# Optimization experiments

Hardware: AMD Instinct MI355X
Metric: run time of the kernel (lower is better)

Reference implementation:

```python
import jax, jax.numpy as jnp
import numpy as np

B, C, H, W = 16, 384, 128, 128
RED = 6                      # reduction
CH = C // RED                # 64
CF = C // 2 + 1              # 193 rfft bins


def setup_inputs() -> dict:
    key = jax.random.key(0)
    ks = jax.random.split(key, 9)
    sc = 0.05
    return {
        "x":   jax.random.normal(ks[0], (B, C, H, W), dtype=jnp.float32),
        "W1":  jax.random.normal(ks[1], (CH, C, 3, 3), dtype=jnp.float32) * sc,
        "b1":  jax.random.normal(ks[2], (CH,), dtype=jnp.float32) * sc,
        "W2":  jax.random.normal(ks[3], (C, CH, 3, 3), dtype=jnp.float32) * sc,
        "b2":  jax.random.normal(ks[4], (C,), dtype=jnp.float32) * sc,
        "Ws1": jax.random.normal(ks[5], (CF, C), dtype=jnp.float32) * sc,
        "bs1": jax.random.normal(ks[6], (CF,), dtype=jnp.float32) * sc,
        "Ws2": jax.random.normal(ks[7], (CF, C), dtype=jnp.float32) * sc,
        "bs2": jax.random.normal(ks[8], (CF,), dtype=jnp.float32) * sc,
    }


def reference(x, W1, b1, W2, b2, Ws1, bs1, Ws2, bs2):
    b, c = x.shape[0], x.shape[1]
    # global average pool -> [b, c]
    y0 = jnp.mean(x, axis=(2, 3))
    # fc: 3x3 convs on 1x1 spatial input (pad=1) reduce to center-tap matmuls
    h = jax.nn.relu(y0 @ W1[:, :, 1, 1].T + b1)            # [b, c//red]
    y = jax.nn.sigmoid(h @ W2[:, :, 1, 1].T + b2)          # [b, c]
    # seq1 / seq2: 1x1 convs on [b, c, 1, 1]
    s1 = jax.nn.relu(y @ Ws1.T + bs1)                      # [b, c//2+1]
    s2 = jax.nn.relu(y @ Ws2.T + bs2)                      # [b, c//2+1]
    # rfft2 over (1, c) spatial dims == 1-D rfft over channel axis
    yf = jnp.fft.rfft(y, axis=-1)                          # [b, c//2+1] complex
    amp = jnp.abs(yf) * s1
    pha = jnp.angle(yf) * s2
    rec = jax.lax.complex(amp * jnp.cos(pha), amp * jnp.sin(pha))
    xr = jnp.fft.irfft(rec, n=c, axis=-1)                  # [b, c]
    out = (xr * y)[:, :, None, None]                       # [b, c, 1, 1]
    return out
```

## Files before the change

### kernel.cpp

```cpp
#include <hip/hip_runtime.h>

#define BB 16
#define CC 384
#define CH 64
#define CF 193
#define HW 16384

__global__ __launch_bounds__(256) void pool_kernel(const float4* __restrict__ x,
                                                   float* __restrict__ y0) {
    const int plane = blockIdx.x;
    const float4* p = x + (size_t)plane * (HW / 4);
    const int t = threadIdx.x;

    float s = 0.f;
#pragma unroll
    for (int r = 0; r < HW / 4 / 256; ++r) {
        float4 v = p[t + 256 * r];
        s += v.x + v.y + v.z + v.w;
    }

#pragma unroll
    for (int off = 32; off > 0; off >>= 1) s += __shfl_down(s, off);

    __shared__ float red[4];
    const int wid = t >> 6, lane = t & 63;
    if (lane == 0) red[wid] = s;
    __syncthreads();
    if (t == 0) {
        float tot = red[0] + red[1] + red[2] + red[3];
        y0[plane] = tot * (1.0f / (float)HW);
    }
}

__global__ __launch_bounds__(384) void head_kernel(
    const float* __restrict__ y0g,
    const float* __restrict__ W1,  const float* __restrict__ b1,
    const float* __restrict__ W2,  const float* __restrict__ b2,
    const float* __restrict__ Ws1, const float* __restrict__ bs1,
    const float* __restrict__ Ws2, const float* __restrict__ bs2,
    float* __restrict__ out)
{
    __shared__ float y0[CC], h[CH], y[CC];
    __shared__ float ct[CC], st[CC];
    __shared__ float rr[CF], ri[CF];

    const int b = blockIdx.x, t = threadIdx.x;

    y0[t] = y0g[b * CC + t];
    {
        float ang = (float)t * (6.283185307179586f / (float)CC);
        float sv, cv;
        sincosf(ang, &sv, &cv);
        st[t] = sv; ct[t] = cv;
    }
    __syncthreads();

    if (t < CH) {
        float acc = b1[t];
        const float* w = W1 + (size_t)t * CC * 9 + 4;
        for (int c = 0; c < CC; ++c) acc += y0[c] * w[c * 9];
        h[t] = fmaxf(acc, 0.f);
    }
    __syncthreads();

    {
        float acc = b2[t];
        const float* w = W2 + (size_t)t * CH * 9 + 4;
        for (int j = 0; j < CH; ++j) acc += h[j] * w[j * 9];
        y[t] = 1.f / (1.f + expf(-acc));
    }
    __syncthreads();

    if (t < CF) {
        const float* w1r = Ws1 + (size_t)t * CC;
        const float* w2r = Ws2 + (size_t)t * CC;
        float a1 = bs1[t], a2 = bs2[t];
        float re = 0.f, im = 0.f;
        int m = 0;
        for (int c = 0; c < CC; ++c) {
            float yc = y[c];
            a1 += yc * w1r[c];
            a2 += yc * w2r[c];
            re += yc * ct[m];
            im -= yc * st[m];
            m += t; if (m >= CC) m -= CC;
        }
        a1 = fmaxf(a1, 0.f);
        a2 = fmaxf(a2, 0.f);
        float amp = sqrtf(re * re + im * im) * a1;
        float pha = atan2f(im, re) * a2;
        float sp, cp;
        sincosf(pha, &sp, &cp);
        rr[t] = amp * cp;
        ri[t] = amp * sp;
    }
    __syncthreads();

    {
        float acc = 0.f;
        int m = 0;
        for (int k = 1; k < 192; ++k) {
            m += t; if (m >= CC) m -= CC;
            acc += rr[k] * ct[m] - ri[k] * st[m];
        }
        float nyq = (t & 1) ? -rr[192] : rr[192];
        float xr = (rr[0] + 2.f * acc + nyq) * (1.0f / (float)CC);
        out[b * CC + t] = xr * y[t];
    }
}

extern "C" void kernel_launch(void* const* d_in, const int* in_sizes, int n_in,
                              void* d_out, int out_size, void* d_ws, size_t ws_size,
                              hipStream_t stream) {
    const float4* x = (const float4*)d_in[0];
    const float* W1  = (const float*)d_in[1];
    const float* b1  = (const float*)d_in[2];
    const float* W2  = (const float*)d_in[3];
    const float* b2  = (const float*)d_in[4];
    const float* Ws1 = (const float*)d_in[5];
    const float* bs1 = (const float*)d_in[6];
    const float* Ws2 = (const float*)d_in[7];
    const float* bs2 = (const float*)d_in[8];
    float* out = (float*)d_out;

    float* y0 = (float*)d_ws;

    pool_kernel<<<BB * CC, 256, 0, stream>>>(x, y0);
    head_kernel<<<BB, 384, 0, stream>>>(y0, W1, b1, W2, b2, Ws1, bs1, Ws2, bs2, out);
}
```

Measured before the change: 614.4 us.

## Split head into batched fc1, fc2, spectral and irfft kernels

Replaces the single per-batch head kernel, which ran only 16 blocks, with four kernels. Each kernel maps batch onto thread lanes and output features onto blocks, so weight rows are shared across the batch. Pooled activations are stored channel-major so batch lanes read contiguously. This is meant to remove the serial latency of the low-parallelism head. In exchange it adds extra kernel launches and global round-trips for the intermediates.

```diff
diff --git a/kernel.cpp b/kernel.cpp
--- a/kernel.cpp
+++ b/kernel.cpp
@@ -6,10 +6,12 @@
 #define CF 193
 #define HW 16384
 
+#define TWO_PI_OVER_CC (6.283185307179586f / (float)CC)
+
 __global__ __launch_bounds__(256) void pool_kernel(const float4* __restrict__ x,
-                                                   float* __restrict__ y0) {
-    const int plane = blockIdx.x;
-    const float4* p = x + (size_t)plane * (HW / 4);
+                                                   float* __restrict__ y0T) {
+    const int c = blockIdx.x, b = blockIdx.y;
+    const float4* p = x + (size_t)(b * CC + c) * (HW / 4);
     const int t = threadIdx.x;
 
     float s = 0.f;
@@ -18,7 +20,6 @@
         float4 v = p[t + 256 * r];
         s += v.x + v.y + v.z + v.w;
     }
-
 #pragma unroll
     for (int off = 32; off > 0; off >>= 1) s += __shfl_down(s, off);
 
@@ -28,91 +29,111 @@
     __syncthreads();
     if (t == 0) {
         float tot = red[0] + red[1] + red[2] + red[3];
-        y0[plane] = tot * (1.0f / (float)HW);
+        y0T[c * BB + b] = tot * (1.0f / (float)HW);
     }
 }
 
-__global__ __launch_bounds__(384) void head_kernel(
-    const float* __restrict__ y0g,
-    const float* __restrict__ W1,  const float* __restrict__ b1,
-    const float* __restrict__ W2,  const float* __restrict__ b2,
-    const float* __restrict__ Ws1, const float* __restrict__ bs1,
-    const float* __restrict__ Ws2, const float* __restrict__ bs2,
-    float* __restrict__ out)
-{
-    __shared__ float y0[CC], h[CH], y[CC];
+__global__ __launch_bounds__(256) void fc1_kernel(const float* __restrict__ y0T,
+                                                  const float* __restrict__ W1,
+                                                  const float* __restrict__ b1,
+                                                  float* __restrict__ hT) {
+    const int t = threadIdx.x;
+    const int b = t & 15;
+    const int j = blockIdx.x * 16 + (t >> 4);
+    const float* w = W1 + (size_t)j * CC * 9 + 4;
+    float acc = b1[j];
+#pragma unroll 4
+    for (int c = 0; c < CC; ++c) acc += y0T[c * BB + b] * w[c * 9];
+    hT[j * BB + b] = fmaxf(acc, 0.f);
+}
+
+__global__ __launch_bounds__(256) void fc2_kernel(const float* __restrict__ hT,
+                                                  const float* __restrict__ W2,
+                                                  const float* __restrict__ b2,
+                                                  float* __restrict__ yT) {
+    const int t = threadIdx.x;
+    const int b = t & 15;
+    const int c = blockIdx.x * 16 + (t >> 4);
+    const float* w = W2 + (size_t)c * CH * 9 + 4;
+    float acc = b2[c];
+#pragma unroll 4
+    for (int j = 0; j < CH; ++j) acc += hT[j * BB + b] * w[j * 9];
+    yT[c * BB + b] = 1.f / (1.f + expf(-acc));
+}
+
+__global__ __launch_bounds__(256) void spec_kernel(const float* __restrict__ yT,
+                                                   const float* __restrict__ Ws1,
+                                                   const float* __restrict__ bs1,
+                                                   const float* __restrict__ Ws2,
+                                                   const float* __restrict__ bs2,
+                                                   float* __restrict__ rr,
+                                                   float* __restrict__ ri) {
     __shared__ float ct[CC], st[CC];
-    __shared__ float rr[CF], ri[CF];
-
-    const int b = blockIdx.x, t = threadIdx.x;
-
-    y0[t] = y0g[b * CC + t];
-    {
-        float ang = (float)t * (6.283185307179586f / (float)CC);
-        float sv, cv;
-        sincosf(ang, &sv, &cv);
-        st[t] = sv; ct[t] = cv;
+    const int t = threadIdx.x;
+    for (int i = t; i < CC; i += 256) {
+        float sv, cv; sincosf((float)i * TWO_PI_OVER_CC, &sv, &cv);
+        ct[i] = cv; st[i] = sv;
     }
     __syncthreads();
 
-    if (t < CH) {
-        float acc = b1[t];
-        const float* w = W1 + (size_t)t * CC * 9 + 4;
-        for (int c = 0; c < CC; ++c) acc += y0[c] * w[c * 9];
-        h[t] = fmaxf(acc, 0.f);
+    const int b = t & 15;
+    const int k = blockIdx.x * 16 + (t >> 4);
+    if (k >= CF) return;
+
+    const float* w1 = Ws1 + (size_t)k * CC;
+    const float* w2 = Ws2 + (size_t)k * CC;
+    float a1 = bs1[k], a2 = bs2[k];
+    float re = 0.f, im = 0.f;
+    int m = 0;
+#pragma unroll 4
+    for (int c = 0; c < CC; ++c) {
+        float yc = yT[c * BB + b];
+        a1 += yc * w1[c];
+        a2 += yc * w2[c];
+        re += yc * ct[m];
+        im -= yc * st[m];
+        m += k; if (m >= CC) m -= CC;
+    }
+    a1 = fmaxf(a1, 0.f);
+    a2 = fmaxf(a2, 0.f);
+    float amp = sqrtf(re * re + im * im) * a1;
+    float pha = atan2f(im, re) * a2;
+    float sp, cp; sincosf(pha, &sp, &cp);
+    rr[k * BB + b] = amp * cp;
+    ri[k * BB + b] = amp * sp;
+}
+
+__global__ __launch_bounds__(256) void irfft_kernel(const float* __restrict__ yT,
+                                                    const float* __restrict__ rr,
+                                                    const float* __restrict__ ri,
+                                                    float* __restrict__ out) {
+    __shared__ float ct[CC], st[CC];
+    const int t = threadIdx.x;
+    for (int i = t; i < CC; i += 256) {
+        float sv, cv; sincosf((float)i * TWO_PI_OVER_CC, &sv, &cv);
+        ct[i] = cv; st[i] = sv;
     }
     __syncthreads();
 
-    {
-        float acc = b2[t];
-        const float* w = W2 + (size_t)t * CH * 9 + 4;
-        for (int j = 0; j < CH; ++j) acc += h[j] * w[j * 9];
-        y[t] = 1.f / (1.f + expf(-acc));
+    const int c = blockIdx.x * 16 + (t & 15);
+    const int b = t >> 4;
+
+    float acc = 0.f;
+    int m = 0;
+#pragma unroll 4
+    for (int k = 1; k < 192; ++k) {
+        m += c; if (m >= CC) m -= CC;
+        acc += rr[k * BB + b] * ct[m] - ri[k * BB + b] * st[m];
     }
-    __syncthreads();
-
-    if (t < CF) {
-        const float* w1r = Ws1 + (size_t)t * CC;
-        const float* w2r = Ws2 + (size_t)t * CC;
-        float a1 = bs1[t], a2 = bs2[t];
-        float re = 0.f, im = 0.f;
-        int m = 0;
-        for (int c = 0; c < CC; ++c) {
-            float yc = y[c];
-            a1 += yc * w1r[c];
-            a2 += yc * w2r[c];
-            re += yc * ct[m];
-            im -= yc * st[m];
-            m += t; if (m >= CC) m -= CC;
-        }
-        a1 = fmaxf(a1, 0.f);
-        a2 = fmaxf(a2, 0.f);
-        float amp = sqrtf(re * re + im * im) * a1;
-        float pha = atan2f(im, re) * a2;
-        float sp, cp;
-        sincosf(pha, &sp, &cp);
-        rr[t] = amp * cp;
-        ri[t] = amp * sp;
-    }
-    __syncthreads();
-
-    {
-        float acc = 0.f;
-        int m = 0;
-        for (int k = 1; k < 192; ++k) {
-            m += t; if (m >= CC) m -= CC;
-            acc += rr[k] * ct[m] - ri[k] * st[m];
-        }
-        float nyq = (t & 1) ? -rr[192] : rr[192];
-        float xr = (rr[0] + 2.f * acc + nyq) * (1.0f / (float)CC);
-        out[b * CC + t] = xr * y[t];
-    }
+    float nyq = (c & 1) ? -rr[192 * BB + b] : rr[192 * BB + b];
+    float xr = (rr[b] + 2.f * acc + nyq) * (1.0f / (float)CC);
+    out[b * CC + c] = xr * yT[c * BB + b];
 }
 
 extern "C" void kernel_launch(void* const* d_in, const int* in_sizes, int n_in,
                               void* d_out, int out_size, void* d_ws, size_t ws_size,
                               hipStream_t stream) {
-    const float4* x = (const float4*)d_in[0];
+    const float4* x  = (const float4*)d_in[0];
     const float* W1  = (const float*)d_in[1];
     const float* b1  = (const float*)d_in[2];
     const float* W2  = (const float*)d_in[3];
@@ -123,8 +144,16 @@
     const float* bs2 = (const float*)d_in[8];
     float* out = (float*)d_out;
 
-    float* y0 = (float*)d_ws;
+    float* ws  = (float*)d_ws;
+    float* y0T = ws;
+    float* hT  = y0T + CC * BB;
+    float* yT  = hT  + CH * BB;
+    float* rr  = yT  + CC * BB;
+    float* ri  = rr  + CF * BB;
 
-    pool_kernel<<<BB * CC, 256, 0, stream>>>(x, y0);
-    head_kernel<<<BB, 384, 0, stream>>>(y0, W1, b1, W2, b2, Ws1, bs1, Ws2, bs2, out);
+    pool_kernel <<<dim3(CC, BB), 256, 0, stream>>>(x, y0T);
+    fc1_kernel  <<<CH / 16,      256, 0, stream>>>(y0T, W1, b1, hT);
+    fc2_kernel  <<<CC / 16,      256, 0, stream>>>(hT, W2, b2, yT);
+    spec_kernel <<<(CF + 15)/16, 256, 0, stream>>>(yT, Ws1, bs1, Ws2, bs2, rr, ri);
+    irfft_kernel<<<CC / 16,      256, 0, stream>>>(yT, rr, ri, out);
 }
```

After: 645.7 us. +5.1%, slower.
